# Optimization experiments

Hardware: AMD Instinct MI355X
Metric: run time of the kernel (lower is better)

The kernel has to match this reference:

```python
import jax, jax.numpy as jnp
import numpy as np

B, S, H, E, D, K = 2, 2048, 2048, 8, 2048, 2


def setup_inputs() -> dict:
    key = jax.random.key(0)
    ks = jax.random.split(key, 4)
    # lecun_normal-style scaling: std = 1/sqrt(fan_in)
    return {
        "x": jax.random.normal(ks[0], (B, S, H), jnp.float32),
        "router_w": jax.random.normal(ks[1], (H, E), jnp.float32) / np.sqrt(H).astype(np.float32),
        "router_b": jnp.zeros((E,), jnp.float32),
        "expert_w": jax.random.normal(ks[2], (E, H, D), jnp.float32) / np.sqrt(H).astype(np.float32),
        "expert_b": jnp.zeros((E, D), jnp.float32),
        "out_w": jax.random.normal(ks[3], (D, D), jnp.float32) / np.sqrt(D).astype(np.float32),
        "out_b": jnp.zeros((D,), jnp.float32),
    }


def reference(x, router_w, router_b, expert_w, expert_b, out_w, out_b):
    num_experts = expert_w.shape[0]
    # Router: logits -> softmax -> top-2 -> renormalize
    router_logits = jnp.einsum("bsh,he->bse", x, router_w) + router_b
    router_probs = jax.nn.softmax(router_logits, axis=-1)
    top_k_probs, top_k_indices = jax.lax.top_k(router_probs, K)  # [B,S,K]
    top_k_probs = top_k_probs / jnp.sum(top_k_probs, axis=-1, keepdims=True)
    # Per-expert gate weight: sum of top-k probs routed to that expert. [B,S,E]
    onehot = jax.nn.one_hot(top_k_indices, num_experts, dtype=x.dtype)  # [B,S,K,E]
    gates = jnp.einsum("bsk,bske->bse", top_k_probs, onehot)
    # Dense per-expert GEMM + gelu (mask-and-multiply MoE; gate==0 kills unrouted tokens)
    expert_out = jax.nn.gelu(jnp.einsum("bsh,ehd->ebsd", x, expert_w) + expert_b[:, None, None, :])
    combined = jnp.einsum("bse,ebsd->bsd", gates, expert_out)
    # Output projection
    return jnp.einsum("bsd,df->bsf", combined, out_w) + out_b
```

## Files before the change

kernel.cpp:

```cpp
#include <hip/hip_runtime.h>
#include <stdint.h>

#define H_DIM 2048
#define E_NUM 8
#define D_DIM 2048
#define NTOK 4096
#define BM 128
#define BN 128
#define BK 32

typedef __bf16 bf16x8 __attribute__((ext_vector_type(8)));
typedef float f32x4 __attribute__((ext_vector_type(4)));

__device__ __forceinline__ unsigned short f2bf(float f) {
    union { float f; uint32_t u; } c; c.f = f;
    uint32_t r = (c.u + 0x7FFFu + ((c.u >> 16) & 1u)) >> 16;
    return (unsigned short)r;
}
__device__ __forceinline__ float bf2f(unsigned short h) {
    union { float f; uint32_t u; } c; c.u = ((uint32_t)h) << 16;
    return c.f;
}

__global__ __launch_bounds__(256) void router_kernel(
    const float* __restrict__ x, const float* __restrict__ rw,
    const float* __restrict__ rb, int* __restrict__ counts,
    uint32_t* __restrict__ tok, float* __restrict__ gate) {
    int t = blockIdx.x;
    const float* xr = x + (size_t)t * H_DIM;
    float p[E_NUM];
#pragma unroll
    for (int e = 0; e < E_NUM; e++) p[e] = 0.f;
    for (int h = threadIdx.x; h < H_DIM; h += 256) {
        float xv = xr[h];
        const float* r = rw + (size_t)h * E_NUM;
#pragma unroll
        for (int e = 0; e < E_NUM; e++) p[e] += xv * r[e];
    }
#pragma unroll
    for (int e = 0; e < E_NUM; e++) {
#pragma unroll
        for (int off = 32; off > 0; off >>= 1) p[e] += __shfl_down(p[e], off, 64);
    }
    __shared__ float red[4][E_NUM];
    int lane = threadIdx.x & 63, w = threadIdx.x >> 6;
    if (lane == 0) {
#pragma unroll
        for (int e = 0; e < E_NUM; e++) red[w][e] = p[e];
    }
    __syncthreads();
    if (threadIdx.x == 0) {
        float l[E_NUM];
#pragma unroll
        for (int e = 0; e < E_NUM; e++)
            l[e] = red[0][e] + red[1][e] + red[2][e] + red[3][e] + rb[e];
        int e0 = 0;
#pragma unroll
        for (int e = 1; e < E_NUM; e++) if (l[e] > l[e0]) e0 = e;
        int e1 = (e0 == 0) ? 1 : 0;
#pragma unroll
        for (int e = 0; e < E_NUM; e++) if (e != e0 && l[e] > l[e1]) e1 = e;
        float g0 = 1.f / (1.f + expf(l[e1] - l[e0]));
        float g1 = 1.f - g0;
        int p0 = atomicAdd(&counts[e0], 1);
        tok[e0 * NTOK + p0] = (uint32_t)t;
        gate[e0 * NTOK + p0] = g0;
        int p1 = atomicAdd(&counts[e1], 1);
        tok[e1 * NTOK + p1] = (uint32_t)t | (1u << 16);
        gate[e1 * NTOK + p1] = g1;
    }
}

__global__ __launch_bounds__(256) void cvt_bf16_kernel(
    const float* __restrict__ src, unsigned short* __restrict__ dst, int n4) {
    int i = blockIdx.x * 256 + threadIdx.x;
    if (i >= n4) return;
    float4 v = ((const float4*)src)[i];
    ushort4 o;
    o.x = f2bf(v.x); o.y = f2bf(v.y); o.z = f2bf(v.z); o.w = f2bf(v.w);
    ((ushort4*)dst)[i] = o;
}

__global__ __launch_bounds__(256) void transpose_cvt_kernel(
    const float* __restrict__ src, unsigned short* __restrict__ dst,
    int K_, int N_) {
    __shared__ unsigned short tile[64][72];
    size_t moff = (size_t)blockIdx.z * (size_t)K_ * N_;
    const float* s = src + moff;
    unsigned short* d = dst + moff;
    int k0 = blockIdx.y * 64, n0 = blockIdx.x * 64;
    int r = threadIdx.x >> 4;
    int c = (threadIdx.x & 15) * 4;
#pragma unroll
    for (int p = 0; p < 4; p++) {
        int k = p * 16 + r;
        float4 v = *(const float4*)(s + (size_t)(k0 + k) * N_ + n0 + c);
        tile[k][c + 0] = f2bf(v.x);
        tile[k][c + 1] = f2bf(v.y);
        tile[k][c + 2] = f2bf(v.z);
        tile[k][c + 3] = f2bf(v.w);
    }
    __syncthreads();
#pragma unroll
    for (int p = 0; p < 4; p++) {
        int n = p * 16 + r;
        ushort4 o;
        o.x = tile[c + 0][n];
        o.y = tile[c + 1][n];
        o.z = tile[c + 2][n];
        o.w = tile[c + 3][n];
        *(ushort4*)(d + (size_t)(n0 + n) * K_ + k0 + c) = o;
    }
}

__global__ __launch_bounds__(256) void expert_gemm_kernel(
    const unsigned short* __restrict__ xb,
    const unsigned short* __restrict__ ewT,
    const float* __restrict__ eb,
    const int* __restrict__ counts,
    const uint32_t* __restrict__ tok,
    const float* __restrict__ gate,
    unsigned short* __restrict__ Y)
{
    int e = blockIdx.z;
    int cnt = counts[e];
    int m0 = blockIdx.y * BM;
    if (m0 >= cnt) return;
    int n0 = blockIdx.x * BN;

    __shared__ unsigned short As[BM][BK + 8];
    __shared__ unsigned short Bs[BN][BK + 8];
    __shared__ uint32_t tok_s[BM];
    __shared__ float gate_s[BM];

    int tid = threadIdx.x;
    if (tid < BM) {
        int idx = m0 + tid;
        uint32_t tk = 0; float g = 0.f;
        if (idx < cnt) { tk = tok[e * NTOK + idx]; g = gate[e * NTOK + idx]; }
        tok_s[tid] = tk; gate_s[tid] = g;
    }
    __syncthreads();

    int ar = tid >> 2;
    int ac = (tid & 3) * 8;
    const unsigned short* ag0 = xb + (size_t)(tok_s[ar] & 0xFFFFu) * H_DIM + ac;
    const unsigned short* ag1 = xb + (size_t)(tok_s[ar + 64] & 0xFFFFu) * H_DIM + ac;
    const unsigned short* bbase = ewT + (size_t)e * D_DIM * H_DIM;
    const unsigned short* bg0 = bbase + (size_t)(n0 + ar) * H_DIM + ac;
    const unsigned short* bg1 = bg0 + (size_t)64 * H_DIM;

    int lane = tid & 63;
    int wave = tid >> 6;
    int wm = (wave >> 1) * 64;
    int wn = (wave & 1) * 64;
    int row16 = lane & 15;
    int quad = lane >> 4;
    int k8 = quad * 8;

    f32x4 acc[4][4];
#pragma unroll
    for (int i = 0; i < 4; i++)
#pragma unroll
        for (int j = 0; j < 4; j++) acc[i][j] = (f32x4)(0.f);

    for (int kk = 0; kk < H_DIM; kk += BK) {
        uint4 a0 = *(const uint4*)(ag0 + kk);
        uint4 a1 = *(const uint4*)(ag1 + kk);
        uint4 b0 = *(const uint4*)(bg0 + kk);
        uint4 b1 = *(const uint4*)(bg1 + kk);
        __syncthreads();
        *(uint4*)&As[ar][ac] = a0;
        *(uint4*)&As[ar + 64][ac] = a1;
        *(uint4*)&Bs[ar][ac] = b0;
        *(uint4*)&Bs[ar + 64][ac] = b1;
        __syncthreads();
        bf16x8 af[4], bff[4];
#pragma unroll
        for (int i = 0; i < 4; i++)
            af[i] = *(const bf16x8*)&As[wm + i * 16 + row16][k8];
#pragma unroll
        for (int j = 0; j < 4; j++)
            bff[j] = *(const bf16x8*)&Bs[wn + j * 16 + row16][k8];
#pragma unroll
        for (int i = 0; i < 4; i++)
#pragma unroll
            for (int j = 0; j < 4; j++)
                acc[i][j] = __builtin_amdgcn_mfma_f32_16x16x32_bf16(
                    af[i], bff[j], acc[i][j], 0, 0, 0);
    }

#pragma unroll
    for (int i = 0; i < 4; i++) {
        int rbase = wm + i * 16 + quad * 4;
#pragma unroll
        for (int j = 0; j < 4; j++) {
            int n = n0 + wn + j * 16 + row16;
            float bias = eb[e * D_DIM + n];
#pragma unroll
            for (int r = 0; r < 4; r++) {
                int lrow = rbase + r;
                if (m0 + lrow < cnt) {
                    uint32_t tk = tok_s[lrow];
                    float g = gate_s[lrow];
                    float v = acc[i][j][r] + bias;
                    float q = 0.7978845608028654f * (v + 0.044715f * v * v * v);
                    float gl = v / (1.f + __expf(-2.f * q));
                    int token = tk & 0xFFFF;
                    int slot = (tk >> 16) & 1;
                    Y[((size_t)token * 2 + slot) * D_DIM + n] = f2bf(g * gl);
                }
            }
        }
    }
}

__global__ __launch_bounds__(256) void combine_kernel(
    const unsigned short* __restrict__ Y, unsigned short* __restrict__ comb) {
    int i = blockIdx.x * 256 + threadIdx.x;
    int t = i >> 8;
    int dc = (i & 255) * 8;
    uint4 u0 = *(const uint4*)(Y + (size_t)t * 2 * D_DIM + dc);
    uint4 u1 = *(const uint4*)(Y + ((size_t)t * 2 + 1) * D_DIM + dc);
    uint4 o;
    uint32_t* po = (uint32_t*)&o;
    const uint32_t* p0 = (const uint32_t*)&u0;
    const uint32_t* p1 = (const uint32_t*)&u1;
#pragma unroll
    for (int k = 0; k < 4; k++) {
        uint32_t a = p0[k], b = p1[k];
        float s0 = bf2f((unsigned short)(a & 0xFFFF)) + bf2f((unsigned short)(b & 0xFFFF));
        float s1 = bf2f((unsigned short)(a >> 16)) + bf2f((unsigned short)(b >> 16));
        po[k] = (uint32_t)f2bf(s0) | ((uint32_t)f2bf(s1) << 16);
    }
    *(uint4*)(comb + (size_t)t * D_DIM + dc) = o;
}

__global__ __launch_bounds__(256) void out_gemm_kernel(
    const unsigned short* __restrict__ comb,
    const unsigned short* __restrict__ owT,
    const float* __restrict__ ob,
    float* __restrict__ out) {
    int m0 = blockIdx.y * BM, n0 = blockIdx.x * BN;
    __shared__ unsigned short As[BM][BK + 8];
    __shared__ unsigned short Bs[BN][BK + 8];
    int tid = threadIdx.x;
    int ar = tid >> 2;
    int ac = (tid & 3) * 8;
    const unsigned short* ag0 = comb + (size_t)(m0 + ar) * D_DIM + ac;
    const unsigned short* ag1 = ag0 + (size_t)64 * D_DIM;
    const unsigned short* bg0 = owT + (size_t)(n0 + ar) * D_DIM + ac;
    const unsigned short* bg1 = bg0 + (size_t)64 * D_DIM;

    int lane = tid & 63;
    int wave = tid >> 6;
    int wm = (wave >> 1) * 64;
    int wn = (wave & 1) * 64;
    int row16 = lane & 15;
    int quad = lane >> 4;
    int k8 = quad * 8;

    f32x4 acc[4][4];
#pragma unroll
    for (int i = 0; i < 4; i++)
#pragma unroll
        for (int j = 0; j < 4; j++) acc[i][j] = (f32x4)(0.f);

    for (int kk = 0; kk < D_DIM; kk += BK) {
        uint4 a0 = *(const uint4*)(ag0 + kk);
        uint4 a1 = *(const uint4*)(ag1 + kk);
        uint4 b0 = *(const uint4*)(bg0 + kk);
        uint4 b1 = *(const uint4*)(bg1 + kk);
        __syncthreads();
        *(uint4*)&As[ar][ac] = a0;
        *(uint4*)&As[ar + 64][ac] = a1;
        *(uint4*)&Bs[ar][ac] = b0;
        *(uint4*)&Bs[ar + 64][ac] = b1;
        __syncthreads();
        bf16x8 af[4], bff[4];
#pragma unroll
        for (int i = 0; i < 4; i++)
            af[i] = *(const bf16x8*)&As[wm + i * 16 + row16][k8];
#pragma unroll
        for (int j = 0; j < 4; j++)
            bff[j] = *(const bf16x8*)&Bs[wn + j * 16 + row16][k8];
#pragma unroll
        for (int i = 0; i < 4; i++)
#pragma unroll
            for (int j = 0; j < 4; j++)
                acc[i][j] = __builtin_amdgcn_mfma_f32_16x16x32_bf16(
                    af[i], bff[j], acc[i][j], 0, 0, 0);
    }

#pragma unroll
    for (int i = 0; i < 4; i++) {
        int rbase = m0 + wm + i * 16 + quad * 4;
#pragma unroll
        for (int j = 0; j < 4; j++) {
            int n = n0 + wn + j * 16 + row16;
            float bias = ob[n];
#pragma unroll
            for (int r = 0; r < 4; r++) {
                out[(size_t)(rbase + r) * D_DIM + n] = acc[i][j][r] + bias;
            }
        }
    }
}

extern "C" void kernel_launch(void* const* d_in, const int* in_sizes, int n_in,
                              void* d_out, int out_size, void* d_ws, size_t ws_size,
                              hipStream_t stream) {
    const float* x        = (const float*)d_in[0];
    const float* router_w = (const float*)d_in[1];
    const float* router_b = (const float*)d_in[2];
    const float* expert_w = (const float*)d_in[3];
    const float* expert_b = (const float*)d_in[4];
    const float* out_w    = (const float*)d_in[5];
    const float* out_b    = (const float*)d_in[6];
    float* out = (float*)d_out;

    char* w = (char*)d_ws;
    int* counts = (int*)w;
    uint32_t* tok = (uint32_t*)(w + 256);
    float* gate = (float*)(w + 256 + E_NUM * NTOK * 4);
    size_t off = 256 + (size_t)2 * E_NUM * NTOK * 4;
    unsigned short* xb = (unsigned short*)(w + off);
    off += (size_t)NTOK * H_DIM * 2;
    unsigned short* ewT = (unsigned short*)(w + off);
    off += (size_t)E_NUM * H_DIM * D_DIM * 2;
    unsigned short* owT = (unsigned short*)(w + off);
    off += (size_t)D_DIM * D_DIM * 2;
    unsigned short* Y = (unsigned short*)(w + off);
    off += (size_t)NTOK * 2 * D_DIM * 2;
    unsigned short* comb = (unsigned short*)(w + off);

    hipMemsetAsync(d_ws, 0, 256, stream);
    router_kernel<<<NTOK, 256, 0, stream>>>(x, router_w, router_b, counts, tok, gate);
    cvt_bf16_kernel<<<(NTOK * H_DIM / 4 + 255) / 256, 256, 0, stream>>>(x, xb, NTOK * H_DIM / 4);
    transpose_cvt_kernel<<<dim3(32, 32, 8), 256, 0, stream>>>(expert_w, ewT, H_DIM, D_DIM);
    transpose_cvt_kernel<<<dim3(32, 32, 1), 256, 0, stream>>>(out_w, owT, D_DIM, D_DIM);
    expert_gemm_kernel<<<dim3(16, 32, 8), 256, 0, stream>>>(xb, ewT, expert_b, counts, tok, gate, Y);
    combine_kernel<<<NTOK * D_DIM / 8 / 256, 256, 0, stream>>>(Y, comb);
    out_gemm_kernel<<<dim3(16, 32), 256, 0, stream>>>(comb, owT, out_b, out);
}
```

Measured before the change: 564.4 us.

## Load GEMM tiles straight to LDS and fuse router with bf16 conversion

Both GEMM kernels now stage A and B tiles with global_load_lds 16-byte direct-to-LDS copies instead of loading into registers and then storing to shared memory. This requires dropping the row padding, so each wave fills 32 contiguous tile rows. Separately, the router becomes one wave per token that also writes the bf16 copy of x, which removes the separate conversion kernel and a second read of x. The trade-off is that unpadded LDS rows may bring bank conflicts on the fragment reads, and the loop still has no multi-buffering to hide the direct loads.

```diff
diff --git a/kernel.cpp b/kernel.cpp
--- a/kernel.cpp
+++ b/kernel.cpp
@@ -22,45 +22,52 @@
     return c.f;
 }
 
-__global__ __launch_bounds__(256) void router_kernel(
+__device__ __forceinline__ void gl_lds16(const unsigned short* g, unsigned short* l) {
+    __builtin_amdgcn_global_load_lds(
+        (const __attribute__((address_space(1))) unsigned int*)g,
+        (__attribute__((address_space(3))) unsigned int*)l, 16, 0, 0);
+}
+
+__global__ __launch_bounds__(256) void router_cvt_kernel(
     const float* __restrict__ x, const float* __restrict__ rw,
     const float* __restrict__ rb, int* __restrict__ counts,
-    uint32_t* __restrict__ tok, float* __restrict__ gate) {
-    int t = blockIdx.x;
+    uint32_t* __restrict__ tok, float* __restrict__ gate,
+    unsigned short* __restrict__ xb) {
+    int t = (blockIdx.x * 256 + threadIdx.x) >> 6;
+    int lane = threadIdx.x & 63;
     const float* xr = x + (size_t)t * H_DIM;
+    unsigned short* xo = xb + (size_t)t * H_DIM;
     float p[E_NUM];
 #pragma unroll
     for (int e = 0; e < E_NUM; e++) p[e] = 0.f;
-    for (int h = threadIdx.x; h < H_DIM; h += 256) {
-        float xv = xr[h];
-        const float* r = rw + (size_t)h * E_NUM;
-#pragma unroll
-        for (int e = 0; e < E_NUM; e++) p[e] += xv * r[e];
+#pragma unroll
+    for (int pass = 0; pass < H_DIM / 256; pass++) {
+        int h = pass * 256 + lane * 4;
+        float4 v = *(const float4*)(xr + h);
+        ushort4 o;
+        o.x = f2bf(v.x); o.y = f2bf(v.y); o.z = f2bf(v.z); o.w = f2bf(v.w);
+        *(ushort4*)(xo + h) = o;
+        const float* r0 = rw + (size_t)h * E_NUM;
+#pragma unroll
+        for (int e = 0; e < E_NUM; e++)
+            p[e] += v.x * r0[e] + v.y * r0[e + 8] + v.z * r0[e + 16] + v.w * r0[e + 24];
     }
 #pragma unroll
     for (int e = 0; e < E_NUM; e++) {
 #pragma unroll
-        for (int off = 32; off > 0; off >>= 1) p[e] += __shfl_down(p[e], off, 64);
-    }
-    __shared__ float red[4][E_NUM];
-    int lane = threadIdx.x & 63, w = threadIdx.x >> 6;
+        for (int off = 1; off < 64; off <<= 1) p[e] += __shfl_xor(p[e], off, 64);
+    }
     if (lane == 0) {
-#pragma unroll
-        for (int e = 0; e < E_NUM; e++) red[w][e] = p[e];
-    }
-    __syncthreads();
-    if (threadIdx.x == 0) {
         float l[E_NUM];
 #pragma unroll
-        for (int e = 0; e < E_NUM; e++)
-            l[e] = red[0][e] + red[1][e] + red[2][e] + red[3][e] + rb[e];
+        for (int e = 0; e < E_NUM; e++) l[e] = p[e] + rb[e];
         int e0 = 0;
 #pragma unroll
         for (int e = 1; e < E_NUM; e++) if (l[e] > l[e0]) e0 = e;
         int e1 = (e0 == 0) ? 1 : 0;
 #pragma unroll
         for (int e = 0; e < E_NUM; e++) if (e != e0 && l[e] > l[e1]) e1 = e;
-        float g0 = 1.f / (1.f + expf(l[e1] - l[e0]));
+        float g0 = 1.f / (1.f + __expf(l[e1] - l[e0]));
         float g1 = 1.f - g0;
         int p0 = atomicAdd(&counts[e0], 1);
         tok[e0 * NTOK + p0] = (uint32_t)t;
@@ -69,16 +76,6 @@
         tok[e1 * NTOK + p1] = (uint32_t)t | (1u << 16);
         gate[e1 * NTOK + p1] = g1;
     }
-}
-
-__global__ __launch_bounds__(256) void cvt_bf16_kernel(
-    const float* __restrict__ src, unsigned short* __restrict__ dst, int n4) {
-    int i = blockIdx.x * 256 + threadIdx.x;
-    if (i >= n4) return;
-    float4 v = ((const float4*)src)[i];
-    ushort4 o;
-    o.x = f2bf(v.x); o.y = f2bf(v.y); o.z = f2bf(v.z); o.w = f2bf(v.w);
-    ((ushort4*)dst)[i] = o;
 }
 
 __global__ __launch_bounds__(256) void transpose_cvt_kernel(
@@ -128,8 +125,8 @@
     if (m0 >= cnt) return;
     int n0 = blockIdx.x * BN;
 
-    __shared__ unsigned short As[BM][BK + 8];
-    __shared__ unsigned short Bs[BN][BK + 8];
+    __shared__ unsigned short As[BM][BK];
+    __shared__ unsigned short Bs[BN][BK];
     __shared__ uint32_t tok_s[BM];
     __shared__ float gate_s[BM];
 
@@ -142,16 +139,22 @@
     }
     __syncthreads();
 
-    int ar = tid >> 2;
-    int ac = (tid & 3) * 8;
-    const unsigned short* ag0 = xb + (size_t)(tok_s[ar] & 0xFFFFu) * H_DIM + ac;
-    const unsigned short* ag1 = xb + (size_t)(tok_s[ar + 64] & 0xFFFFu) * H_DIM + ac;
-    const unsigned short* bbase = ewT + (size_t)e * D_DIM * H_DIM;
-    const unsigned short* bg0 = bbase + (size_t)(n0 + ar) * H_DIM + ac;
-    const unsigned short* bg1 = bg0 + (size_t)64 * H_DIM;
-
     int lane = tid & 63;
     int wave = tid >> 6;
+    int sr = lane >> 2;
+    int sc = (lane & 3) * 8;
+    int r0 = wave * 32 + sr;
+    int r1 = wave * 32 + 16 + sr;
+    const unsigned short* agp0 = xb + (size_t)(tok_s[r0] & 0xFFFFu) * H_DIM + sc;
+    const unsigned short* agp1 = xb + (size_t)(tok_s[r1] & 0xFFFFu) * H_DIM + sc;
+    const unsigned short* bbase = ewT + (size_t)e * D_DIM * H_DIM;
+    const unsigned short* bgp0 = bbase + (size_t)(n0 + r0) * H_DIM + sc;
+    const unsigned short* bgp1 = bbase + (size_t)(n0 + r1) * H_DIM + sc;
+    unsigned short* la0 = &As[wave * 32][0];
+    unsigned short* la1 = &As[wave * 32 + 16][0];
+    unsigned short* lb0 = &Bs[wave * 32][0];
+    unsigned short* lb1 = &Bs[wave * 32 + 16][0];
+
     int wm = (wave >> 1) * 64;
     int wn = (wave & 1) * 64;
     int row16 = lane & 15;
@@ -165,15 +168,11 @@
         for (int j = 0; j < 4; j++) acc[i][j] = (f32x4)(0.f);
 
     for (int kk = 0; kk < H_DIM; kk += BK) {
-        uint4 a0 = *(const uint4*)(ag0 + kk);
-        uint4 a1 = *(const uint4*)(ag1 + kk);
-        uint4 b0 = *(const uint4*)(bg0 + kk);
-        uint4 b1 = *(const uint4*)(bg1 + kk);
         __syncthreads();
-        *(uint4*)&As[ar][ac] = a0;
-        *(uint4*)&As[ar + 64][ac] = a1;
-        *(uint4*)&Bs[ar][ac] = b0;
-        *(uint4*)&Bs[ar + 64][ac] = b1;
+        gl_lds16(agp0 + kk, la0);
+        gl_lds16(agp1 + kk, la1);
+        gl_lds16(bgp0 + kk, lb0);
+        gl_lds16(bgp1 + kk, lb1);
         __syncthreads();
         bf16x8 af[4], bff[4];
 #pragma unroll
@@ -242,18 +241,24 @@
     const float* __restrict__ ob,
     float* __restrict__ out) {
     int m0 = blockIdx.y * BM, n0 = blockIdx.x * BN;
-    __shared__ unsigned short As[BM][BK + 8];
-    __shared__ unsigned short Bs[BN][BK + 8];
+    __shared__ unsigned short As[BM][BK];
+    __shared__ unsigned short Bs[BN][BK];
     int tid = threadIdx.x;
-    int ar = tid >> 2;
-    int ac = (tid & 3) * 8;
-    const unsigned short* ag0 = comb + (size_t)(m0 + ar) * D_DIM + ac;
-    const unsigned short* ag1 = ag0 + (size_t)64 * D_DIM;
-    const unsigned short* bg0 = owT + (size_t)(n0 + ar) * D_DIM + ac;
-    const unsigned short* bg1 = bg0 + (size_t)64 * D_DIM;
-
     int lane = tid & 63;
     int wave = tid >> 6;
+    int sr = lane >> 2;
+    int sc = (lane & 3) * 8;
+    int r0 = wave * 32 + sr;
+    int r1 = wave * 32 + 16 + sr;
+    const unsigned short* agp0 = comb + (size_t)(m0 + r0) * D_DIM + sc;
+    const unsigned short* agp1 = comb + (size_t)(m0 + r1) * D_DIM + sc;
+    const unsigned short* bgp0 = owT + (size_t)(n0 + r0) * D_DIM + sc;
+    const unsigned short* bgp1 = owT + (size_t)(n0 + r1) * D_DIM + sc;
+    unsigned short* la0 = &As[wave * 32][0];
+    unsigned short* la1 = &As[wave * 32 + 16][0];
+    unsigned short* lb0 = &Bs[wave * 32][0];
+    unsigned short* lb1 = &Bs[wave * 32 + 16][0];
+
     int wm = (wave >> 1) * 64;
     int wn = (wave & 1) * 64;
     int row16 = lane & 15;
@@ -267,15 +272,11 @@
         for (int j = 0; j < 4; j++) acc[i][j] = (f32x4)(0.f);
 
     for (int kk = 0; kk < D_DIM; kk += BK) {
-        uint4 a0 = *(const uint4*)(ag0 + kk);
-        uint4 a1 = *(const uint4*)(ag1 + kk);
-        uint4 b0 = *(const uint4*)(bg0 + kk);
-        uint4 b1 = *(const uint4*)(bg1 + kk);
         __syncthreads();
-        *(uint4*)&As[ar][ac] = a0;
-        *(uint4*)&As[ar + 64][ac] = a1;
-        *(uint4*)&Bs[ar][ac] = b0;
-        *(uint4*)&Bs[ar + 64][ac] = b1;
+        gl_lds16(agp0 + kk, la0);
+        gl_lds16(agp1 + kk, la1);
+        gl_lds16(bgp0 + kk, lb0);
+        gl_lds16(bgp1 + kk, lb1);
         __syncthreads();
         bf16x8 af[4], bff[4];
 #pragma unroll
@@ -335,8 +336,8 @@
     unsigned short* comb = (unsigned short*)(w + off);
 
     hipMemsetAsync(d_ws, 0, 256, stream);
-    router_kernel<<<NTOK, 256, 0, stream>>>(x, router_w, router_b, counts, tok, gate);
-    cvt_bf16_kernel<<<(NTOK * H_DIM / 4 + 255) / 256, 256, 0, stream>>>(x, xb, NTOK * H_DIM / 4);
+    router_cvt_kernel<<<NTOK / 4, 256, 0, stream>>>(x, router_w, router_b,
+                                                    counts, tok, gate, xb);
     transpose_cvt_kernel<<<dim3(32, 32, 8), 256, 0, stream>>>(expert_w, ewT, H_DIM, D_DIM);
     transpose_cvt_kernel<<<dim3(32, 32, 1), 256, 0, stream>>>(out_w, owT, D_DIM, D_DIM);
     expert_gemm_kernel<<<dim3(16, 32, 8), 256, 0, stream>>>(xb, ewT, expert_b, counts, tok, gate, Y);
```

Measured after the change: 534.7 us. 1.06x faster.
